# Kernel optimization log

Hardware: AMD Instinct MI355X
Metric: run time of the kernel (lower is better)

## Reference

```python
import jax, jax.numpy as jnp
import numpy as np

N_NODES = 50000
N_EDGES = 800000
IN_F, E_F, OUT_F = 128, 32, 128

def setup_inputs() -> dict:
    key = jax.random.key(0)
    ks = jax.random.split(key, 8)
    return {
        "h": jax.random.normal(ks[0], (N_NODES, IN_F), dtype=jnp.float32),
        "eftr": jax.random.normal(ks[1], (N_EDGES, E_F), dtype=jnp.float32),
        "weight": jax.random.normal(ks[2], (IN_F + E_F, OUT_F), dtype=jnp.float32) * (1.0 / np.sqrt(IN_F + E_F)),
        "W_w": jax.random.normal(ks[3], (OUT_F, IN_F + OUT_F), dtype=jnp.float32) * (1.0 / np.sqrt(IN_F + OUT_F)),
        "W_b": jax.random.normal(ks[4], (OUT_F,), dtype=jnp.float32) * 0.01,
        "bias": jnp.zeros((OUT_F,), dtype=jnp.float32),
        "src_idx": jax.random.randint(ks[5], (N_EDGES,), 0, N_NODES, dtype=jnp.int64) if jax.config.jax_enable_x64 else jax.random.randint(ks[5], (N_EDGES,), 0, N_NODES, dtype=jnp.int32),
        "dst_idx": jax.random.randint(ks[6], (N_EDGES,), 0, N_NODES, dtype=jnp.int32),
        "num_dst": N_NODES,
    }

def reference(h, eftr, weight, W_w, W_b, bias, src_idx, dst_idx, num_dst):
    # Segment-mean of concat([h[src], eftr]) over dst neighborhoods.
    # Sum node part and edge part separately (avoids materializing the concat mailbox).
    sum_h = jax.ops.segment_sum(h[src_idx], dst_idx, num_segments=num_dst)   # [D, IN_F]
    sum_e = jax.ops.segment_sum(eftr, dst_idx, num_segments=num_dst)        # [D, E_F]
    cnt = jax.ops.segment_sum(jnp.ones((dst_idx.shape[0],), h.dtype), dst_idx, num_segments=num_dst)
    denom = jnp.maximum(cnt, 1.0)[:, None]  # zero-degree nodes -> h_neigh = 0
    feat_mean = jnp.concatenate([sum_h / denom, sum_e / denom], axis=-1)    # [D, IN_F+E_F]
    h_neigh = feat_mean @ weight                                            # [D, OUT_F]
    h_dst = h[:num_dst]
    h_prime = jnp.concatenate([h_dst, h_neigh], axis=1) @ W_w.T + W_b       # Linear W
    h_prime = h_prime + bias
    return h_prime
```

## Files before the change

### kernel.cpp

```cpp
#include <hip/hip_runtime.h>

#define NN   50000
#define NE   800000
#define INF  128
#define EF   32
#define OUTF 128
#define KDIM 288
#define NBLK ((NN + 1023) / 1024)
#define CVT_BLKS 3125

typedef __attribute__((ext_vector_type(8))) short     short8;
typedef __attribute__((ext_vector_type(8))) unsigned short ushort8;
typedef __attribute__((ext_vector_type(4))) float     float4v;
typedef __attribute__((ext_vector_type(2))) float     float2v;

__device__ __forceinline__ unsigned short f2bf(float f) {
    union { float f; unsigned int u; } c; c.f = f;
    const unsigned int r = (c.u + 0x7FFFu + ((c.u >> 16) & 1u)) >> 16;
    return (unsigned short)r;
}

__global__ void prep_kernel(const float* __restrict__ weight,
                            const float* __restrict__ W_w,
                            const float* __restrict__ W_b,
                            const float* __restrict__ bias,
                            float* __restrict__ Mmat,
                            float* __restrict__ cvec) {
    __shared__ float wrow[OUTF];
    const int r = blockIdx.x;
    const int j = threadIdx.x;
    if (r < 128) {
        Mmat[r * OUTF + j] = W_w[j * 256 + r];
        return;
    }
    if (r == KDIM) {
        cvec[j] = W_b[j] + bias[j];
        return;
    }
    const int m = r - 128;
    wrow[j] = weight[m * OUTF + j];
    __syncthreads();
    float acc = 0.f;
#pragma unroll 8
    for (int k = 0; k < OUTF; ++k)
        acc += wrow[k] * W_w[j * 256 + 128 + k];
    Mmat[r * OUTF + j] = acc;
}

__global__ void pack_kernel(const float* __restrict__ Mmat,
                            unsigned short* __restrict__ Mb) {
    const int b = blockIdx.x;
    const int kb = b >> 3;
    const int ct = b & 7;
    const int lane = threadIdx.x;
    const int col = ct * 16 + (lane & 15);
    const int k0 = kb * 32 + (lane >> 4) * 8;
    ushort8 v;
#pragma unroll
    for (int i = 0; i < 8; ++i)
        v[i] = f2bf(Mmat[(size_t)(k0 + i) * OUTF + col]);
    *(ushort8*)(Mb + ((size_t)(b * 64 + lane) * 8)) = v;
}

__global__ __launch_bounds__(256)
void cvt_hist_kernel(const float* __restrict__ h,
                     unsigned short* __restrict__ hb,
                     const int* __restrict__ dst,
                     int* __restrict__ off,
                     int* __restrict__ rank) {
    const int b = blockIdx.x;
    if (b < CVT_BLKS) {
        const size_t i = (size_t)(b * 256 + threadIdx.x) * 8;
        const float4 a0 = *(const float4*)(h + i);
        const float4 a1 = *(const float4*)(h + i + 4);
        ushort8 v;
        v[0] = f2bf(a0.x); v[1] = f2bf(a0.y); v[2] = f2bf(a0.z); v[3] = f2bf(a0.w);
        v[4] = f2bf(a1.x); v[5] = f2bf(a1.y); v[6] = f2bf(a1.z); v[7] = f2bf(a1.w);
        *(ushort8*)(hb + i) = v;
        return;
    }
    if (b == CVT_BLKS) {
        if (threadIdx.x < 16) {
            ushort8 z = {};
            *(ushort8*)(hb + (size_t)NN * INF + threadIdx.x * 8) = z;
        }
        return;
    }
    const int e = ((b - CVT_BLKS - 1) * 256 + threadIdx.x) * 4;
    if (e < NE) {
        const int4 d = *(const int4*)(dst + e);
        int4 r;
        r.x = atomicAdd(&off[d.x], 1);
        r.y = atomicAdd(&off[d.y], 1);
        r.z = atomicAdd(&off[d.z], 1);
        r.w = atomicAdd(&off[d.w], 1);
        *(int4*)(rank + e) = r;
    }
}

__global__ __launch_bounds__(256)
void scan1_kernel(const int* __restrict__ off, int* __restrict__ partial) {
    const int b = blockIdx.x;
    const int tid = threadIdx.x;
    const int idx = b * 1024 + tid * 4;
    int v0 = 0, v1 = 0, v2 = 0, v3 = 0;
    if (idx + 3 < NN) {
        const int4 q = *(const int4*)(off + idx);
        v0 = q.x; v1 = q.y; v2 = q.z; v3 = q.w;
    } else {
        if (idx + 0 < NN) v0 = off[idx + 0];
        if (idx + 1 < NN) v1 = off[idx + 1];
        if (idx + 2 < NN) v2 = off[idx + 2];
    }
    int t = v0 + v1 + v2 + v3;
#pragma unroll
    for (int ofs = 32; ofs > 0; ofs >>= 1) t += __shfl_down(t, ofs);
    __shared__ int wsum[4];
    if ((tid & 63) == 0) wsum[tid >> 6] = t;
    __syncthreads();
    if (tid == 0) partial[b] = wsum[0] + wsum[1] + wsum[2] + wsum[3];
}

__global__ __launch_bounds__(256)
void scan3_kernel(int* __restrict__ off, const int* __restrict__ partial) {
    __shared__ int blockbase;
    __shared__ int wsum[4];
    const int b = blockIdx.x;
    const int tid = threadIdx.x;
    const int lane = tid & 63;
    const int wid = tid >> 6;

    if (b == 0 && tid == 0) off[NN] = NE;

    if (wid == 0) {
        const int v = (lane < NBLK) ? partial[lane] : 0;
        int x = v;
#pragma unroll
        for (int ofs = 1; ofs < 64; ofs <<= 1) {
            const int t = __shfl_up(x, ofs);
            if (lane >= ofs) x += t;
        }
        if (lane == b) blockbase = x - v;
    }

    const int idx = b * 1024 + tid * 4;
    int v0 = 0, v1 = 0, v2 = 0, v3 = 0;
    if (idx + 3 < NN) {
        const int4 q = *(const int4*)(off + idx);
        v0 = q.x; v1 = q.y; v2 = q.z; v3 = q.w;
    } else {
        if (idx + 0 < NN) v0 = off[idx + 0];
        if (idx + 1 < NN) v1 = off[idx + 1];
        if (idx + 2 < NN) v2 = off[idx + 2];
    }
    const int tsum = v0 + v1 + v2 + v3;
    int x = tsum;
#pragma unroll
    for (int ofs = 1; ofs < 64; ofs <<= 1) {
        const int t = __shfl_up(x, ofs);
        if (lane >= ofs) x += t;
    }
    if (lane == 63) wsum[wid] = x;
    __syncthreads();
    int wp = 0;
    for (int w = 0; w < wid; ++w) wp += wsum[w];
    const int base = blockbase + wp + (x - tsum);
    if (idx + 0 < NN) off[idx + 0] = base;
    if (idx + 1 < NN) off[idx + 1] = base + v0;
    if (idx + 2 < NN) off[idx + 2] = base + v0 + v1;
    if (idx + 3 < NN) off[idx + 3] = base + v0 + v1 + v2;
}

__global__ __launch_bounds__(256)
void scatter_ids_kernel(const int* __restrict__ srcv,
                        const int* __restrict__ dst,
                        const int* __restrict__ off,
                        const int* __restrict__ rank,
                        int2* __restrict__ eo2) {
    const int e = (blockIdx.x * 256 + threadIdx.x) * 4;
    if (e < NE) {
        const int4 s = *(const int4*)(srcv + e);
        const int4 d = *(const int4*)(dst + e);
        const int4 r = *(const int4*)(rank + e);
        eo2[off[d.x] + r.x] = make_int2(s.x, e + 0);
        eo2[off[d.y] + r.y] = make_int2(s.y, e + 1);
        eo2[off[d.z] + r.z] = make_int2(s.z, e + 2);
        eo2[off[d.w] + r.w] = make_int2(s.w, e + 3);
    }
}

__global__ __launch_bounds__(256)
void gather_kernel(const unsigned short* __restrict__ hb,
                   const float* __restrict__ eftr,
                   const int* __restrict__ off,
                   const int2* __restrict__ eo2,
                   unsigned short* __restrict__ mean_h,
                   unsigned short* __restrict__ mean_e) {
    const int tid = threadIdx.x;
    const int lane = tid & 63;
    const int node = blockIdx.x * 4 + (tid >> 6);
    if (node >= NN) return;

    const int start = off[node];
    const int end   = off[node + 1];

    const int ql = lane & 15;
    const int qg = lane >> 4;

    float ax[8] = {0.f, 0.f, 0.f, 0.f, 0.f, 0.f, 0.f, 0.f};
    float aex = 0.f, aey = 0.f;

    for (int base = start; base < end; base += 64) {
        const int m = min(64, end - base);
        int px = 0, py = 0;
        if (lane < m) {
            const long long pv =
                __builtin_nontemporal_load((const long long*)(eo2 + base + lane));
            px = (int)pv;
            py = (int)(pv >> 32);
        }
        for (int j = 0; j < m; j += 8) {
#pragma unroll
            for (int u = 0; u < 2; ++u) {
                const int eidx = j + u * 4 + qg;
                const bool valid = eidx < m;
                const int bidx = (eidx & 63) * 4;
                int s = __builtin_amdgcn_ds_bpermute(bidx, px);
                int e = __builtin_amdgcn_ds_bpermute(bidx, py);
                s = valid ? s : NN;
                e = valid ? e : 0;

                const uint4 hv = *(const uint4*)(hb + (size_t)s * INF + ql * 8);
#pragma unroll
                for (int k = 0; k < 4; ++k) {
                    const unsigned w = (&hv.x)[k];
                    union { unsigned u; float f; } lo, hi;
                    lo.u = w << 16;
                    hi.u = w & 0xffff0000u;
                    ax[2 * k]     += lo.f;
                    ax[2 * k + 1] += hi.f;
                }

                const float2v ev = __builtin_nontemporal_load(
                    (const float2v*)(eftr + (size_t)e * EF + ql * 2));
                aex += valid ? ev.x : 0.f;
                aey += valid ? ev.y : 0.f;
            }
        }
    }

#pragma unroll
    for (int k = 0; k < 8; ++k) {
        ax[k] += __shfl_xor(ax[k], 16);
        ax[k] += __shfl_xor(ax[k], 32);
    }
    aex += __shfl_xor(aex, 16); aex += __shfl_xor(aex, 32);
    aey += __shfl_xor(aey, 16); aey += __shfl_xor(aey, 32);

    if (qg == 0) {
        const float inv = 1.f / fmaxf((float)(end - start), 1.f);
        ushort8 mv;
#pragma unroll
        for (int k = 0; k < 8; ++k) mv[k] = f2bf(ax[k] * inv);
        *(ushort8*)(mean_h + (size_t)node * INF + ql * 8) = mv;
        const unsigned me =
            (unsigned)f2bf(aex * inv) | ((unsigned)f2bf(aey * inv) << 16);
        *(unsigned*)(mean_e + (size_t)node * EF + ql * 2) = me;
    }
}

__global__ __launch_bounds__(256)
void node_gemm_kernel(const unsigned short* __restrict__ hb,
                      const unsigned short* __restrict__ mean_h,
                      const unsigned short* __restrict__ mean_e,
                      const unsigned short* __restrict__ Mb,
                      const float* __restrict__ cvec,
                      float* __restrict__ out) {
    const int tid = threadIdx.x;
    const int lane = tid & 63;
    const int wid = tid >> 6;
    const int nt = blockIdx.x * 4 + wid;
    const int m16 = lane & 15;
    const int quad = lane >> 4;
    const int koff = quad * 8;

    const int anode = nt * 16 + m16;
    const int nclamp = (anode < NN) ? anode : (NN - 1);

    float4v acc[8] = {};

    for (int kb = 0; kb < 9; ++kb) {
        const unsigned short* srcp;
        if (kb < 4)
            srcp = hb + (size_t)nclamp * INF + kb * 32 + koff;
        else if (kb < 8)
            srcp = mean_h + (size_t)nclamp * INF + (kb - 4) * 32 + koff;
        else
            srcp = mean_e + (size_t)nclamp * EF + koff;
        const short8 a = *(const short8*)(const void*)srcp;

        const short8* bp = (const short8*)(Mb + (size_t)kb * 8 * 64 * 8);
#pragma unroll
        for (int ct = 0; ct < 8; ++ct) {
            const short8 b = bp[ct * 64 + lane];
            acc[ct] = __builtin_amdgcn_mfma_f32_16x16x32_bf16(a, b, acc[ct], 0, 0, 0);
        }
    }

    float cv[8];
#pragma unroll
    for (int ct = 0; ct < 8; ++ct) cv[ct] = cvec[ct * 16 + m16];

#pragma unroll
    for (int r = 0; r < 4; ++r) {
        const int nrow = nt * 16 + quad * 4 + r;
        if (nrow < NN) {
            float* orow = out + (size_t)nrow * OUTF;
#pragma unroll
            for (int ct = 0; ct < 8; ++ct)
                __builtin_nontemporal_store(acc[ct][r] + cv[ct],
                                            &orow[ct * 16 + m16]);
        }
    }
}

extern "C" void kernel_launch(void* const* d_in, const int* in_sizes, int n_in,
                              void* d_out, int out_size, void* d_ws, size_t ws_size,
                              hipStream_t stream) {
    const float* h      = (const float*)d_in[0];
    const float* eftr   = (const float*)d_in[1];
    const float* weight = (const float*)d_in[2];
    const float* W_w    = (const float*)d_in[3];
    const float* W_b    = (const float*)d_in[4];
    const float* bias   = (const float*)d_in[5];
    const int*   src    = (const int*)d_in[6];
    const int*   dst    = (const int*)d_in[7];
    float* out = (float*)d_out;

    char* base = (char*)d_ws;
    unsigned short* mean_h = (unsigned short*)(base);
    unsigned short* mean_e = (unsigned short*)(base + 12800000);
    unsigned short* h_bf   = (unsigned short*)(base + 16000000);
    float* Mmat            = (float*)(base + 28800512);
    float* cvec            = (float*)(base + 28947968);
    unsigned short* Mb     = (unsigned short*)(base + 28948480);
    int*   off             = (int*)(base + 29022208);
    int2*  eo2             = (int2*)(base + 29222912);
    int*   rank            = (int*)(base + 35622912);
    int*   partial         = (int*)(base + 38822912);

    hipMemsetAsync(off, 0, (size_t)NN * sizeof(int), stream);

    prep_kernel<<<KDIM + 1, 128, 0, stream>>>(weight, W_w, W_b, bias, Mmat, cvec);
    pack_kernel<<<72, 64, 0, stream>>>(Mmat, Mb);
    cvt_hist_kernel<<<CVT_BLKS + 1 + (NE / 4 + 255) / 256, 256, 0, stream>>>(
        h, h_bf, dst, off, rank);
    scan1_kernel<<<NBLK, 256, 0, stream>>>(off, partial);
    scan3_kernel<<<NBLK, 256, 0, stream>>>(off, partial);
    scatter_ids_kernel<<<(NE / 4 + 255) / 256, 256, 0, stream>>>(src, dst, off,
                                                                 rank, eo2);
    gather_kernel<<<(NN + 3) / 4, 256, 0, stream>>>(h_bf, eftr, off, eo2,
                                                    mean_h, mean_e);
    node_gemm_kernel<<<(NN / 64) + 1, 256, 0, stream>>>(h_bf, mean_h, mean_e,
                                                        Mb, cvec, out);
}
```

Before: 289.4 us.

## Fuse neighbor gather with node GEMM via LDS and merge weight prep into pack

The segment-mean gather and the output GEMM now run in one kernel. Each block aggregates 16 nodes into a bf16 LDS tile and then runs MFMA over those rows, so the mean_h/mean_e intermediates are never written to or read back from global memory. Separately, the prep and pack kernels are merged so the folded weight matrix is computed and packed directly to bf16, which removes one launch and the fp32 Mmat buffer. In exchange, each wave now gathers four nodes serially before a block barrier, and each wave produces only 2 of the 8 output column tiles. That may lower latency hiding, and load imbalance across nodes can stall the barrier.

```diff
diff --git a/kernel.cpp b/kernel.cpp
--- a/kernel.cpp
+++ b/kernel.cpp
@@ -8,6 +8,7 @@
 #define KDIM 288
 #define NBLK ((NN + 1023) / 1024)
 #define CVT_BLKS 3125
+#define LDS_STRIDE 184
 
 typedef __attribute__((ext_vector_type(8))) short     short8;
 typedef __attribute__((ext_vector_type(8))) unsigned short ushort8;
@@ -20,45 +21,45 @@
     return (unsigned short)r;
 }
 
-__global__ void prep_kernel(const float* __restrict__ weight,
+__global__ void pack_kernel(const float* __restrict__ weight,
                             const float* __restrict__ W_w,
-                            const float* __restrict__ W_b,
-                            const float* __restrict__ bias,
-                            float* __restrict__ Mmat,
-                            float* __restrict__ cvec) {
-    __shared__ float wrow[OUTF];
-    const int r = blockIdx.x;
-    const int j = threadIdx.x;
-    if (r < 128) {
-        Mmat[r * OUTF + j] = W_w[j * 256 + r];
-        return;
-    }
-    if (r == KDIM) {
-        cvec[j] = W_b[j] + bias[j];
-        return;
-    }
-    const int m = r - 128;
-    wrow[j] = weight[m * OUTF + j];
-    __syncthreads();
-    float acc = 0.f;
-#pragma unroll 8
-    for (int k = 0; k < OUTF; ++k)
-        acc += wrow[k] * W_w[j * 256 + 128 + k];
-    Mmat[r * OUTF + j] = acc;
-}
-
-__global__ void pack_kernel(const float* __restrict__ Mmat,
                             unsigned short* __restrict__ Mb) {
+    __shared__ float wrow[32][129];
+    __shared__ float wcol[16][129];
     const int b = blockIdx.x;
     const int kb = b >> 3;
     const int ct = b & 7;
     const int lane = threadIdx.x;
-    const int col = ct * 16 + (lane & 15);
-    const int k0 = kb * 32 + (lane >> 4) * 8;
+    const int colLoc = lane & 15;
+    const int quad = lane >> 4;
+    const int col = ct * 16 + colLoc;
+
     ushort8 v;
-#pragma unroll
-    for (int i = 0; i < 8; ++i)
-        v[i] = f2bf(Mmat[(size_t)(k0 + i) * OUTF + col]);
+    if (kb < 4) {
+        const int k0 = kb * 32 + quad * 8;
+        const float4 p0 = *(const float4*)(W_w + (size_t)col * 256 + k0);
+        const float4 p1 = *(const float4*)(W_w + (size_t)col * 256 + k0 + 4);
+        v[0] = f2bf(p0.x); v[1] = f2bf(p0.y); v[2] = f2bf(p0.z); v[3] = f2bf(p0.w);
+        v[4] = f2bf(p1.x); v[5] = f2bf(p1.y); v[6] = f2bf(p1.z); v[7] = f2bf(p1.w);
+    } else {
+        const int m0 = (kb - 4) * 32;
+        for (int idx = lane; idx < 32 * 128; idx += 64)
+            wrow[idx >> 7][idx & 127] =
+                weight[(size_t)(m0 + (idx >> 7)) * 128 + (idx & 127)];
+        for (int idx = lane; idx < 16 * 128; idx += 64)
+            wcol[idx >> 7][idx & 127] =
+                W_w[(size_t)(ct * 16 + (idx >> 7)) * 256 + 128 + (idx & 127)];
+        __syncthreads();
+        float acc[8] = {};
+        for (int c = 0; c < 128; ++c) {
+            const float wc = wcol[colLoc][c];
+#pragma unroll
+            for (int i = 0; i < 8; ++i)
+                acc[i] += wrow[quad * 8 + i][c] * wc;
+        }
+#pragma unroll
+        for (int i = 0; i < 8; ++i) v[i] = f2bf(acc[i]);
+    }
     *(ushort8*)(Mb + ((size_t)(b * 64 + lane) * 8)) = v;
 }
 
@@ -190,137 +191,126 @@
 }
 
 __global__ __launch_bounds__(256)
-void gather_kernel(const unsigned short* __restrict__ hb,
-                   const float* __restrict__ eftr,
-                   const int* __restrict__ off,
-                   const int2* __restrict__ eo2,
-                   unsigned short* __restrict__ mean_h,
-                   unsigned short* __restrict__ mean_e) {
-    const int tid = threadIdx.x;
-    const int lane = tid & 63;
-    const int node = blockIdx.x * 4 + (tid >> 6);
-    if (node >= NN) return;
-
-    const int start = off[node];
-    const int end   = off[node + 1];
-
-    const int ql = lane & 15;
-    const int qg = lane >> 4;
-
-    float ax[8] = {0.f, 0.f, 0.f, 0.f, 0.f, 0.f, 0.f, 0.f};
-    float aex = 0.f, aey = 0.f;
-
-    for (int base = start; base < end; base += 64) {
-        const int m = min(64, end - base);
-        int px = 0, py = 0;
-        if (lane < m) {
-            const long long pv =
-                __builtin_nontemporal_load((const long long*)(eo2 + base + lane));
-            px = (int)pv;
-            py = (int)(pv >> 32);
-        }
-        for (int j = 0; j < m; j += 8) {
-#pragma unroll
-            for (int u = 0; u < 2; ++u) {
-                const int eidx = j + u * 4 + qg;
-                const bool valid = eidx < m;
-                const int bidx = (eidx & 63) * 4;
-                int s = __builtin_amdgcn_ds_bpermute(bidx, px);
-                int e = __builtin_amdgcn_ds_bpermute(bidx, py);
-                s = valid ? s : NN;
-                e = valid ? e : 0;
-
-                const uint4 hv = *(const uint4*)(hb + (size_t)s * INF + ql * 8);
-#pragma unroll
-                for (int k = 0; k < 4; ++k) {
-                    const unsigned w = (&hv.x)[k];
-                    union { unsigned u; float f; } lo, hi;
-                    lo.u = w << 16;
-                    hi.u = w & 0xffff0000u;
-                    ax[2 * k]     += lo.f;
-                    ax[2 * k + 1] += hi.f;
-                }
-
-                const float2v ev = __builtin_nontemporal_load(
-                    (const float2v*)(eftr + (size_t)e * EF + ql * 2));
-                aex += valid ? ev.x : 0.f;
-                aey += valid ? ev.y : 0.f;
-            }
-        }
-    }
-
-#pragma unroll
-    for (int k = 0; k < 8; ++k) {
-        ax[k] += __shfl_xor(ax[k], 16);
-        ax[k] += __shfl_xor(ax[k], 32);
-    }
-    aex += __shfl_xor(aex, 16); aex += __shfl_xor(aex, 32);
-    aey += __shfl_xor(aey, 16); aey += __shfl_xor(aey, 32);
-
-    if (qg == 0) {
-        const float inv = 1.f / fmaxf((float)(end - start), 1.f);
-        ushort8 mv;
-#pragma unroll
-        for (int k = 0; k < 8; ++k) mv[k] = f2bf(ax[k] * inv);
-        *(ushort8*)(mean_h + (size_t)node * INF + ql * 8) = mv;
-        const unsigned me =
-            (unsigned)f2bf(aex * inv) | ((unsigned)f2bf(aey * inv) << 16);
-        *(unsigned*)(mean_e + (size_t)node * EF + ql * 2) = me;
-    }
-}
-
-__global__ __launch_bounds__(256)
-void node_gemm_kernel(const unsigned short* __restrict__ hb,
-                      const unsigned short* __restrict__ mean_h,
-                      const unsigned short* __restrict__ mean_e,
-                      const unsigned short* __restrict__ Mb,
-                      const float* __restrict__ cvec,
-                      float* __restrict__ out) {
+void gather_gemm_kernel(const unsigned short* __restrict__ hb,
+                        const float* __restrict__ eftr,
+                        const int* __restrict__ off,
+                        const int2* __restrict__ eo2,
+                        const unsigned short* __restrict__ Mb,
+                        const float* __restrict__ W_b,
+                        const float* __restrict__ bias,
+                        float* __restrict__ out) {
+    __shared__ unsigned short ldsA[16 * LDS_STRIDE];
     const int tid = threadIdx.x;
     const int lane = tid & 63;
     const int wid = tid >> 6;
-    const int nt = blockIdx.x * 4 + wid;
+    const int blk = blockIdx.x;
+
+    const int ql = lane & 15;
+    const int qg = lane >> 4;
+
+    for (int i = 0; i < 4; ++i) {
+        const int nloc = wid * 4 + i;
+        const int node = blk * 16 + nloc;
+        const int start = off[node];
+        const int end   = off[node + 1];
+
+        float ax[8] = {0.f, 0.f, 0.f, 0.f, 0.f, 0.f, 0.f, 0.f};
+        float aex = 0.f, aey = 0.f;
+
+        for (int base = start; base < end; base += 64) {
+            const int m = min(64, end - base);
+            int px = 0, py = 0;
+            if (lane < m) {
+                const long long pv =
+                    __builtin_nontemporal_load((const long long*)(eo2 + base + lane));
+                px = (int)pv;
+                py = (int)(pv >> 32);
+            }
+            for (int j = 0; j < m; j += 8) {
+#pragma unroll
+                for (int u = 0; u < 2; ++u) {
+                    const int eidx = j + u * 4 + qg;
+                    const bool valid = eidx < m;
+                    const int bidx = (eidx & 63) * 4;
+                    int s = __builtin_amdgcn_ds_bpermute(bidx, px);
+                    int e = __builtin_amdgcn_ds_bpermute(bidx, py);
+                    s = valid ? s : NN;
+                    e = valid ? e : 0;
+
+                    const uint4 hv = *(const uint4*)(hb + (size_t)s * INF + ql * 8);
+#pragma unroll
+                    for (int k = 0; k < 4; ++k) {
+                        const unsigned w = (&hv.x)[k];
+                        union { unsigned u; float f; } lo, hi;
+                        lo.u = w << 16;
+                        hi.u = w & 0xffff0000u;
+                        ax[2 * k]     += lo.f;
+                        ax[2 * k + 1] += hi.f;
+                    }
+
+                    const float2v ev = __builtin_nontemporal_load(
+                        (const float2v*)(eftr + (size_t)e * EF + ql * 2));
+                    aex += valid ? ev.x : 0.f;
+                    aey += valid ? ev.y : 0.f;
+                }
+            }
+        }
+
+#pragma unroll
+        for (int k = 0; k < 8; ++k) {
+            ax[k] += __shfl_xor(ax[k], 16);
+            ax[k] += __shfl_xor(ax[k], 32);
+        }
+        aex += __shfl_xor(aex, 16); aex += __shfl_xor(aex, 32);
+        aey += __shfl_xor(aey, 16); aey += __shfl_xor(aey, 32);
+
+        if (qg == 0) {
+            const float inv = 1.f / fmaxf((float)(end - start), 1.f);
+            ushort8 mv;
+#pragma unroll
+            for (int k = 0; k < 8; ++k) mv[k] = f2bf(ax[k] * inv);
+            *(ushort8*)(ldsA + nloc * LDS_STRIDE + ql * 8) = mv;
+            const unsigned me =
+                (unsigned)f2bf(aex * inv) | ((unsigned)f2bf(aey * inv) << 16);
+            *(unsigned*)(ldsA + nloc * LDS_STRIDE + 128 + ql * 2) = me;
+        }
+    }
+    __syncthreads();
+
     const int m16 = lane & 15;
     const int quad = lane >> 4;
     const int koff = quad * 8;
-
-    const int anode = nt * 16 + m16;
-    const int nclamp = (anode < NN) ? anode : (NN - 1);
-
-    float4v acc[8] = {};
+    const int ct0 = wid * 2;
+
+    float4v acc0 = {};
+    float4v acc1 = {};
 
     for (int kb = 0; kb < 9; ++kb) {
-        const unsigned short* srcp;
+        short8 a;
         if (kb < 4)
-            srcp = hb + (size_t)nclamp * INF + kb * 32 + koff;
-        else if (kb < 8)
-            srcp = mean_h + (size_t)nclamp * INF + (kb - 4) * 32 + koff;
+            a = *(const short8*)(const void*)(hb + (size_t)(blk * 16 + m16) * INF +
+                                              kb * 32 + koff);
         else
-            srcp = mean_e + (size_t)nclamp * EF + koff;
-        const short8 a = *(const short8*)(const void*)srcp;
-
+            a = *(const short8*)(const void*)(ldsA + m16 * LDS_STRIDE +
+                                              (kb - 4) * 32 + koff);
         const short8* bp = (const short8*)(Mb + (size_t)kb * 8 * 64 * 8);
-#pragma unroll
-        for (int ct = 0; ct < 8; ++ct) {
-            const short8 b = bp[ct * 64 + lane];
-            acc[ct] = __builtin_amdgcn_mfma_f32_16x16x32_bf16(a, b, acc[ct], 0, 0, 0);
-        }
-    }
-
-    float cv[8];
-#pragma unroll
-    for (int ct = 0; ct < 8; ++ct) cv[ct] = cvec[ct * 16 + m16];
+        const short8 b0 = bp[ct0 * 64 + lane];
+        const short8 b1 = bp[(ct0 + 1) * 64 + lane];
+        acc0 = __builtin_amdgcn_mfma_f32_16x16x32_bf16(a, b0, acc0, 0, 0, 0);
+        acc1 = __builtin_amdgcn_mfma_f32_16x16x32_bf16(a, b1, acc1, 0, 0, 0);
+    }
+
+    const int c0 = ct0 * 16 + m16;
+    const int c1 = c0 + 16;
+    const float cv0 = W_b[c0] + bias[c0];
+    const float cv1 = W_b[c1] + bias[c1];
 
 #pragma unroll
     for (int r = 0; r < 4; ++r) {
-        const int nrow = nt * 16 + quad * 4 + r;
-        if (nrow < NN) {
-            float* orow = out + (size_t)nrow * OUTF;
-#pragma unroll
-            for (int ct = 0; ct < 8; ++ct)
-                __builtin_nontemporal_store(acc[ct][r] + cv[ct],
-                                            &orow[ct * 16 + m16]);
-        }
+        const int row = blk * 16 + quad * 4 + r;
+        float* orow = out + (size_t)row * OUTF;
+        __builtin_nontemporal_store(acc0[r] + cv0, &orow[c0]);
+        __builtin_nontemporal_store(acc1[r] + cv1, &orow[c1]);
     }
 }
 
@@ -338,29 +328,22 @@
     float* out = (float*)d_out;
 
     char* base = (char*)d_ws;
-    unsigned short* mean_h = (unsigned short*)(base);
-    unsigned short* mean_e = (unsigned short*)(base + 12800000);
-    unsigned short* h_bf   = (unsigned short*)(base + 16000000);
-    float* Mmat            = (float*)(base + 28800512);
-    float* cvec            = (float*)(base + 28947968);
-    unsigned short* Mb     = (unsigned short*)(base + 28948480);
-    int*   off             = (int*)(base + 29022208);
-    int2*  eo2             = (int2*)(base + 29222912);
-    int*   rank            = (int*)(base + 35622912);
-    int*   partial         = (int*)(base + 38822912);
+    unsigned short* h_bf = (unsigned short*)(base);
+    unsigned short* Mb   = (unsigned short*)(base + 12800512);
+    int*   off           = (int*)(base + 12874752);
+    int2*  eo2           = (int2*)(base + 13075456);
+    int*   rank          = (int*)(base + 19475456);
+    int*   partial       = (int*)(base + 22675456);
 
     hipMemsetAsync(off, 0, (size_t)NN * sizeof(int), stream);
 
-    prep_kernel<<<KDIM + 1, 128, 0, stream>>>(weight, W_w, W_b, bias, Mmat, cvec);
-    pack_kernel<<<72, 64, 0, stream>>>(Mmat, Mb);
+    pack_kernel<<<72, 64, 0, stream>>>(weight, W_w, Mb);
     cvt_hist_kernel<<<CVT_BLKS + 1 + (NE / 4 + 255) / 256, 256, 0, stream>>>(
         h, h_bf, dst, off, rank);
     scan1_kernel<<<NBLK, 256, 0, stream>>>(off, partial);
     scan3_kernel<<<NBLK, 256, 0, stream>>>(off, partial);
     scatter_ids_kernel<<<(NE / 4 + 255) / 256, 256, 0, stream>>>(src, dst, off,
                                                                  rank, eo2);
-    gather_kernel<<<(NN + 3) / 4, 256, 0, stream>>>(h_bf, eftr, off, eo2,
-                                                    mean_h, mean_e);
-    node_gemm_kernel<<<(NN / 64) + 1, 256, 0, stream>>>(h_bf, mean_h, mean_e,
-                                                        Mb, cvec, out);
-}
+    gather_gemm_kernel<<<NN / 16, 256, 0, stream>>>(h_bf, eftr, off, eo2,
+                                                    Mb, W_b, bias, out);
+}
```

Result: slower. 297.6 us (+2.8%).

## Fuse weight prep into pack kernel and simplify gather edge loop

Applied to the files above, without the earlier changes.

The separate prep kernel and the fp32 Mmat intermediate are removed. The pack kernel now computes the folded weight product directly in shared memory and packs it to bf16. The bias add is folded into the GEMM epilogue. The gather loop drops the 64-edge ds_bpermute broadcast and has each lane load its int2 edge pair directly, with four edges per quad-group per iteration. This removes one launch and an intermediate buffer, but adds redundant small loads of edge ids and runs a heavier per-block matmul in the pack kernel using only 72 blocks.

```diff
diff --git a/kernel.cpp b/kernel.cpp
--- a/kernel.cpp
+++ b/kernel.cpp
@@ -5,7 +5,6 @@
 #define INF  128
 #define EF   32
 #define OUTF 128
-#define KDIM 288
 #define NBLK ((NN + 1023) / 1024)
 #define CVT_BLKS 3125
 
@@ -20,45 +19,45 @@
     return (unsigned short)r;
 }
 
-__global__ void prep_kernel(const float* __restrict__ weight,
+__global__ void pack_kernel(const float* __restrict__ weight,
                             const float* __restrict__ W_w,
-                            const float* __restrict__ W_b,
-                            const float* __restrict__ bias,
-                            float* __restrict__ Mmat,
-                            float* __restrict__ cvec) {
-    __shared__ float wrow[OUTF];
-    const int r = blockIdx.x;
-    const int j = threadIdx.x;
-    if (r < 128) {
-        Mmat[r * OUTF + j] = W_w[j * 256 + r];
-        return;
-    }
-    if (r == KDIM) {
-        cvec[j] = W_b[j] + bias[j];
-        return;
-    }
-    const int m = r - 128;
-    wrow[j] = weight[m * OUTF + j];
-    __syncthreads();
-    float acc = 0.f;
-#pragma unroll 8
-    for (int k = 0; k < OUTF; ++k)
-        acc += wrow[k] * W_w[j * 256 + 128 + k];
-    Mmat[r * OUTF + j] = acc;
-}
-
-__global__ void pack_kernel(const float* __restrict__ Mmat,
                             unsigned short* __restrict__ Mb) {
+    __shared__ float wrow[32][129];
+    __shared__ float wcol[16][129];
     const int b = blockIdx.x;
     const int kb = b >> 3;
     const int ct = b & 7;
     const int lane = threadIdx.x;
-    const int col = ct * 16 + (lane & 15);
-    const int k0 = kb * 32 + (lane >> 4) * 8;
+    const int colLoc = lane & 15;
+    const int quad = lane >> 4;
+    const int col = ct * 16 + colLoc;
+
     ushort8 v;
-#pragma unroll
-    for (int i = 0; i < 8; ++i)
-        v[i] = f2bf(Mmat[(size_t)(k0 + i) * OUTF + col]);
+    if (kb < 4) {
+        const int k0 = kb * 32 + quad * 8;
+        const float4 p0 = *(const float4*)(W_w + (size_t)col * 256 + k0);
+        const float4 p1 = *(const float4*)(W_w + (size_t)col * 256 + k0 + 4);
+        v[0] = f2bf(p0.x); v[1] = f2bf(p0.y); v[2] = f2bf(p0.z); v[3] = f2bf(p0.w);
+        v[4] = f2bf(p1.x); v[5] = f2bf(p1.y); v[6] = f2bf(p1.z); v[7] = f2bf(p1.w);
+    } else {
+        const int m0 = (kb - 4) * 32;
+        for (int idx = lane; idx < 32 * 128; idx += 64)
+            wrow[idx >> 7][idx & 127] =
+                weight[(size_t)(m0 + (idx >> 7)) * 128 + (idx & 127)];
+        for (int idx = lane; idx < 16 * 128; idx += 64)
+            wcol[idx >> 7][idx & 127] =
+                W_w[(size_t)(ct * 16 + (idx >> 7)) * 256 + 128 + (idx & 127)];
+        __syncthreads();
+        float acc[8] = {};
+        for (int c = 0; c < 128; ++c) {
+            const float wc = wcol[colLoc][c];
+#pragma unroll
+            for (int i = 0; i < 8; ++i)
+                acc[i] += wrow[quad * 8 + i][c] * wc;
+        }
+#pragma unroll
+        for (int i = 0; i < 8; ++i) v[i] = f2bf(acc[i]);
+    }
     *(ushort8*)(Mb + ((size_t)(b * 64 + lane) * 8)) = v;
 }
 
@@ -210,42 +209,30 @@
     float ax[8] = {0.f, 0.f, 0.f, 0.f, 0.f, 0.f, 0.f, 0.f};
     float aex = 0.f, aey = 0.f;
 
-    for (int base = start; base < end; base += 64) {
-        const int m = min(64, end - base);
-        int px = 0, py = 0;
-        if (lane < m) {
-            const long long pv =
-                __builtin_nontemporal_load((const long long*)(eo2 + base + lane));
-            px = (int)pv;
-            py = (int)(pv >> 32);
-        }
-        for (int j = 0; j < m; j += 8) {
-#pragma unroll
-            for (int u = 0; u < 2; ++u) {
-                const int eidx = j + u * 4 + qg;
-                const bool valid = eidx < m;
-                const int bidx = (eidx & 63) * 4;
-                int s = __builtin_amdgcn_ds_bpermute(bidx, px);
-                int e = __builtin_amdgcn_ds_bpermute(bidx, py);
-                s = valid ? s : NN;
-                e = valid ? e : 0;
-
-                const uint4 hv = *(const uint4*)(hb + (size_t)s * INF + ql * 8);
-#pragma unroll
-                for (int k = 0; k < 4; ++k) {
-                    const unsigned w = (&hv.x)[k];
-                    union { unsigned u; float f; } lo, hi;
-                    lo.u = w << 16;
-                    hi.u = w & 0xffff0000u;
-                    ax[2 * k]     += lo.f;
-                    ax[2 * k + 1] += hi.f;
-                }
-
-                const float2v ev = __builtin_nontemporal_load(
-                    (const float2v*)(eftr + (size_t)e * EF + ql * 2));
-                aex += valid ? ev.x : 0.f;
-                aey += valid ? ev.y : 0.f;
+    for (int j = start; j < end; j += 16) {
+#pragma unroll
+        for (int u = 0; u < 4; ++u) {
+            const int eidx = j + u * 4 + qg;
+            const bool valid = eidx < end;
+            const int2 se = eo2[valid ? eidx : (end - 1)];
+            const int s = valid ? se.x : NN;
+            const int e = se.y;
+
+            const uint4 hv = *(const uint4*)(hb + (size_t)s * INF + ql * 8);
+#pragma unroll
+            for (int k = 0; k < 4; ++k) {
+                const unsigned w = (&hv.x)[k];
+                union { unsigned u; float f; } lo, hi;
+                lo.u = w << 16;
+                hi.u = w & 0xffff0000u;
+                ax[2 * k]     += lo.f;
+                ax[2 * k + 1] += hi.f;
             }
+
+            const float2v ev = __builtin_nontemporal_load(
+                (const float2v*)(eftr + (size_t)e * EF + ql * 2));
+            aex += valid ? ev.x : 0.f;
+            aey += valid ? ev.y : 0.f;
         }
     }
 
@@ -274,7 +261,8 @@
                       const unsigned short* __restrict__ mean_h,
                       const unsigned short* __restrict__ mean_e,
                       const unsigned short* __restrict__ Mb,
-                      const float* __restrict__ cvec,
+                      const float* __restrict__ W_b,
+                      const float* __restrict__ bias,
                       float* __restrict__ out) {
     const int tid = threadIdx.x;
     const int lane = tid & 63;
@@ -309,7 +297,10 @@
 
     float cv[8];
 #pragma unroll
-    for (int ct = 0; ct < 8; ++ct) cv[ct] = cvec[ct * 16 + m16];
+    for (int ct = 0; ct < 8; ++ct) {
+        const int c = ct * 16 + m16;
+        cv[ct] = W_b[c] + bias[c];
+    }
 
 #pragma unroll
     for (int r = 0; r < 4; ++r) {
@@ -341,18 +332,15 @@
     unsigned short* mean_h = (unsigned short*)(base);
     unsigned short* mean_e = (unsigned short*)(base + 12800000);
     unsigned short* h_bf   = (unsigned short*)(base + 16000000);
-    float* Mmat            = (float*)(base + 28800512);
-    float* cvec            = (float*)(base + 28947968);
-    unsigned short* Mb     = (unsigned short*)(base + 28948480);
-    int*   off             = (int*)(base + 29022208);
-    int2*  eo2             = (int2*)(base + 29222912);
-    int*   rank            = (int*)(base + 35622912);
-    int*   partial         = (int*)(base + 38822912);
+    unsigned short* Mb     = (unsigned short*)(base + 28800512);
+    int*   off             = (int*)(base + 28874240);
+    int2*  eo2             = (int2*)(base + 29074944);
+    int*   rank            = (int*)(base + 35474944);
+    int*   partial         = (int*)(base + 38674944);
 
     hipMemsetAsync(off, 0, (size_t)NN * sizeof(int), stream);
 
-    prep_kernel<<<KDIM + 1, 128, 0, stream>>>(weight, W_w, W_b, bias, Mmat, cvec);
-    pack_kernel<<<72, 64, 0, stream>>>(Mmat, Mb);
+    pack_kernel<<<72, 64, 0, stream>>>(weight, W_w, Mb);
     cvt_hist_kernel<<<CVT_BLKS + 1 + (NE / 4 + 255) / 256, 256, 0, stream>>>(
         h, h_bf, dst, off, rank);
     scan1_kernel<<<NBLK, 256, 0, stream>>>(off, partial);
@@ -362,5 +350,5 @@
     gather_kernel<<<(NN + 3) / 4, 256, 0, stream>>>(h_bf, eftr, off, eo2,
                                                     mean_h, mean_e);
     node_gemm_kernel<<<(NN / 64) + 1, 256, 0, stream>>>(h_bf, mean_h, mean_e,
-                                                        Mb, cvec, out);
-}
+                                                        Mb, W_b, bias, out);
+}
```

Result: slower. 302.4 us (+4.5%).

## Restructure gather so each lane owns two feature columns across all edges

Applied to the files above, without the earlier changes.

The gather kernel now maps one wavefront lane to two bf16 columns of the node feature row and walks edges serially, broadcasting indices with readlane instead of ds_bpermute. This removes the cross-lane shuffle reduction at the end and the per-edge predication, and shrinks accumulator registers. Each load becomes a 4-byte access per lane (a 256-byte coalesced row per edge) instead of 16-byte loads covering four edges at once. Edge features are split across the two half-waves, and eight edges are batched per iteration to keep several loads in flight. Partial edge-feature sums from the two half-waves are combined at the end with a single shuffle.

```diff
diff --git a/kernel.cpp b/kernel.cpp
--- a/kernel.cpp
+++ b/kernel.cpp
@@ -204,11 +204,10 @@
     const int start = off[node];
     const int end   = off[node + 1];
 
-    const int ql = lane & 15;
-    const int qg = lane >> 4;
-
-    float ax[8] = {0.f, 0.f, 0.f, 0.f, 0.f, 0.f, 0.f, 0.f};
-    float aex = 0.f, aey = 0.f;
+    float ax = 0.f, ay = 0.f, ae = 0.f;
+    const unsigned short* hcol = hb + lane * 2;
+    const int el = lane & 31;
+    const bool lowhalf = (lane < 32);
 
     for (int base = start; base < end; base += 64) {
         const int m = min(64, end - base);
@@ -219,54 +218,52 @@
             px = (int)pv;
             py = (int)(pv >> 32);
         }
-        for (int j = 0; j < m; j += 8) {
-#pragma unroll
-            for (int u = 0; u < 2; ++u) {
-                const int eidx = j + u * 4 + qg;
-                const bool valid = eidx < m;
-                const int bidx = (eidx & 63) * 4;
-                int s = __builtin_amdgcn_ds_bpermute(bidx, px);
-                int e = __builtin_amdgcn_ds_bpermute(bidx, py);
-                s = valid ? s : NN;
-                e = valid ? e : 0;
-
-                const uint4 hv = *(const uint4*)(hb + (size_t)s * INF + ql * 8);
-#pragma unroll
-                for (int k = 0; k < 4; ++k) {
-                    const unsigned w = (&hv.x)[k];
-                    union { unsigned u; float f; } lo, hi;
-                    lo.u = w << 16;
-                    hi.u = w & 0xffff0000u;
-                    ax[2 * k]     += lo.f;
-                    ax[2 * k + 1] += hi.f;
-                }
-
-                const float2v ev = __builtin_nontemporal_load(
-                    (const float2v*)(eftr + (size_t)e * EF + ql * 2));
-                aex += valid ? ev.x : 0.f;
-                aey += valid ? ev.y : 0.f;
+        int j = 0;
+        for (; j + 7 < m; j += 8) {
+            int s[8], e[8];
+#pragma unroll
+            for (int u = 0; u < 8; ++u) {
+                s[u] = __builtin_amdgcn_readlane(px, j + u);
+                e[u] = __builtin_amdgcn_readlane(py, j + u);
             }
-        }
-    }
-
-#pragma unroll
-    for (int k = 0; k < 8; ++k) {
-        ax[k] += __shfl_xor(ax[k], 16);
-        ax[k] += __shfl_xor(ax[k], 32);
-    }
-    aex += __shfl_xor(aex, 16); aex += __shfl_xor(aex, 32);
-    aey += __shfl_xor(aey, 16); aey += __shfl_xor(aey, 32);
-
-    if (qg == 0) {
-        const float inv = 1.f / fmaxf((float)(end - start), 1.f);
-        ushort8 mv;
-#pragma unroll
-        for (int k = 0; k < 8; ++k) mv[k] = f2bf(ax[k] * inv);
-        *(ushort8*)(mean_h + (size_t)node * INF + ql * 8) = mv;
-        const unsigned me =
-            (unsigned)f2bf(aex * inv) | ((unsigned)f2bf(aey * inv) << 16);
-        *(unsigned*)(mean_e + (size_t)node * EF + ql * 2) = me;
-    }
+            unsigned v[8];
+#pragma unroll
+            for (int u = 0; u < 8; ++u)
+                v[u] = *(const unsigned*)(hcol + (size_t)s[u] * INF);
+            float f[4];
+#pragma unroll
+            for (int u = 0; u < 4; ++u) {
+                const int ee = lowhalf ? e[2 * u] : e[2 * u + 1];
+                f[u] = __builtin_nontemporal_load(&eftr[(size_t)ee * EF + el]);
+            }
+#pragma unroll
+            for (int u = 0; u < 8; ++u) {
+                union { unsigned u; float f; } lo, hi;
+                lo.u = v[u] << 16;
+                hi.u = v[u] & 0xffff0000u;
+                ax += lo.f; ay += hi.f;
+            }
+            ae += (f[0] + f[1]) + (f[2] + f[3]);
+        }
+        for (; j < m; ++j) {
+            const int s0 = __builtin_amdgcn_readlane(px, j);
+            const int e0 = __builtin_amdgcn_readlane(py, j);
+            const unsigned v0 = *(const unsigned*)(hcol + (size_t)s0 * INF);
+            union { unsigned u; float f; } lo, hi;
+            lo.u = v0 << 16;
+            hi.u = v0 & 0xffff0000u;
+            ax += lo.f; ay += hi.f;
+            if (lowhalf) ae += __builtin_nontemporal_load(&eftr[(size_t)e0 * EF + el]);
+        }
+    }
+
+    ae += __shfl(ae, lane + 32);
+
+    const float inv = 1.f / fmaxf((float)(end - start), 1.f);
+    const unsigned mx = f2bf(ax * inv);
+    const unsigned my = f2bf(ay * inv);
+    *(unsigned*)(mean_h + (size_t)node * INF + lane * 2) = mx | (my << 16);
+    if (lowhalf) mean_e[(size_t)node * EF + el] = f2bf(ae * inv);
 }
 
 __global__ __launch_bounds__(256)
```

New measurement: 294.2 us. Within noise of the previous version (+1.7%).
